# Kernel tuning notes

Measured on AMD Instinct MI355X. Metric: run time of the kernel, lower is better.

The kernel has to match this reference:

```python
import jax, jax.numpy as jnp
import numpy as np

B = 2
G = 256            # bev grid size per axis at this stride
STRIDE = 2
PAD = 2
EMB = 128
NPF = 64           # num_pos_feats = emb_dim // 2
LR = np.array([-51.2, -51.2, -3.0, 51.2, 51.2, 1.0], np.float32)
VS = np.array([0.2, 0.2], np.float32)
OFFSET = -128      # round(lr_min / (voxel * stride))
SQRT_DIM = float(np.sqrt(EMB))
Q = 65536
V = B * G * G


def pos2posemb2d(pos, num_pos_feats=NPF, temperature=10000.0):
    # standard interleaved sin/cos 2d position embedding (y first, then x)
    pos = pos * (2.0 * np.pi)
    dim_t = jnp.arange(num_pos_feats, dtype=jnp.float32)
    dim_t = temperature ** (2.0 * (dim_t // 2) / num_pos_feats)
    px = pos[..., 0:1] / dim_t
    py = pos[..., 1:2] / dim_t
    px = jnp.stack((jnp.sin(px[..., 0::2]), jnp.cos(px[..., 1::2])), axis=-1).reshape(pos.shape[0], -1)
    py = jnp.stack((jnp.sin(py[..., 0::2]), jnp.cos(py[..., 1::2])), axis=-1).reshape(pos.shape[0], -1)
    return jnp.concatenate((py, px), axis=-1)


def mlp(x, w1, b1, w2, b2):
    return jax.nn.relu(x @ w1 + b1) @ w2 + b2


def setup_inputs():
    key = jax.random.key(0)
    ks = jax.random.split(key, 16)
    # dense BEV grid of value centers -> value_map scatter is collision-free
    idx = jnp.arange(V)
    b = idx // (G * G)
    x = (idx % (G * G)) // G
    y = idx % G
    ctr_coor = jnp.stack([b, (x - 128) * STRIDE, (y - 128) * STRIDE], axis=-1).astype(jnp.int32)
    ctr_feat = jax.random.normal(ks[0], (V, EMB), jnp.float32)
    bq = jax.random.randint(ks[1], (Q,), 0, B).astype(jnp.float32)
    xy = jax.random.uniform(ks[2], (Q, 2), jnp.float32, -51.0, 51.0)
    ref_pts = jnp.concatenate([bq[:, None], xy], axis=1)
    s = 0.02
    p = lambda k, sh: jax.random.normal(k, sh, jnp.float32) * s
    return dict(
        ref_pts=ref_pts, ctr_coor=ctr_coor, ctr_feat=ctr_feat,
        q_w1=p(ks[3], (EMB, 2 * EMB)), q_b1=jnp.zeros((2 * EMB,), jnp.float32),
        q_w2=p(ks[4], (2 * EMB, EMB)), q_b2=jnp.zeros((EMB,), jnp.float32),
        v_w1=p(ks[5], (EMB, 2 * EMB)), v_b1=jnp.zeros((2 * EMB,), jnp.float32),
        v_w2=p(ks[6], (2 * EMB, EMB)), v_b2=jnp.zeros((EMB,), jnp.float32),
        se_wr=p(ks[7], (EMB, EMB)), se_br=jnp.zeros((EMB,), jnp.float32),
        se_we=p(ks[8], (EMB, EMB)), se_be=jnp.zeros((EMB,), jnp.float32),
    )


def _forward(ref_pts, ctr_feat, q_w1, q_b1, q_w2, q_b2, v_w1, v_b1, v_w2, v_b2,
             se_wr, se_br, se_we, se_be, ctr_coor):
    nv = ctr_feat.shape[0]
    lr = jnp.asarray(LR)
    vs = jnp.asarray(VS)
    # indices2metric: voxel center positions in meters
    ctr_xy = (ctr_coor[:, 1:].astype(jnp.float32) + 0.5) * vs
    # coor_to_indices: grid indices at current stride
    ctr_inds = ctr_coor[:, 1:] // STRIDE - OFFSET                 # (V,2) in [0,G)
    ref_coor = jnp.floor(ref_pts[:, 1:] / vs)                     # metric2indices
    ref_inds = (ref_coor / STRIDE - OFFSET).astype(jnp.int32)     # (Q,2) in [0,G)
    # normalized positions in [0,1]
    qp = (ref_pts[:, 1:] - lr[0:2]) / (lr[3:5] - lr[0:2])
    vp = (ctr_xy - lr[0:2]) / (lr[3:5] - lr[0:2])
    qpos = mlp(pos2posemb2d(qp), q_w1, q_b1, q_w2, q_b2)          # (Q,d)
    vpos = mlp(pos2posemb2d(vp), v_w1, v_b1, v_w2, v_b2)          # (V,d)
    # SELayer_Linear: gate value pos-emb by features
    gate = jax.nn.sigmoid(jax.nn.relu(ctr_feat @ se_wr + se_br) @ se_we + se_be)
    vpos = vpos * gate
    # build padded index map and gather 3x3 neighborhoods
    vmap_grid = -jnp.ones((B, G + 2 * PAD, G + 2 * PAD), jnp.int32)
    vmap_grid = vmap_grid.at[ctr_coor[:, 0], ctr_inds[:, 0] + PAD, ctr_inds[:, 1] + PAD].set(
        jnp.arange(nv, dtype=jnp.int32))
    r = jnp.arange(-1, 2)
    nbrs = jnp.stack(jnp.meshgrid(r, r, indexing='ij'), axis=-1).reshape(-1, 2)  # (9,2)
    bq = ref_pts[:, 0].astype(jnp.int32)
    nx = ref_inds[:, 0:1] + PAD + nbrs[:, 0]                      # (Q,9)
    ny = ref_inds[:, 1:2] + PAD + nbrs[:, 1]
    v_idx = vmap_grid[bq[:, None], nx, ny] + 1                    # missing -> 0 (padded zero row)
    vpos_pad = jnp.concatenate([jnp.zeros((1, EMB), vpos.dtype), vpos], axis=0)
    feat_pad = jnp.concatenate([jnp.zeros((1, EMB), ctr_feat.dtype), ctr_feat], axis=0)
    score = jnp.einsum('qd,qnd->qn', qpos, vpos_pad[v_idx]) / SQRT_DIM
    attn = jax.nn.softmax(score, axis=-1)
    return jnp.einsum('qn,qnd->qd', attn, feat_pad[v_idx])       # (Q,d)


def reference(ref_pts, ctr_coor, ctr_feat, q_w1, q_b1, q_w2, q_b2,
              v_w1, v_b1, v_w2, v_b2, se_wr, se_br, se_we, se_be):
    return _forward(ref_pts, ctr_feat, q_w1, q_b1, q_w2, q_b2,
                    v_w1, v_b1, v_w2, v_b2, se_wr, se_br, se_we, se_be, ctr_coor)
```

## Files before the change

### kernel.cpp

```cpp
#include <hip/hip_runtime.h>
#include <math.h>

#define TWO_PI 6.28318530717958647692f
#define SCALE_INV_SQRT_D 0.08838834764831844f

#define NQ 65536
#define NV 131072

typedef __attribute__((ext_vector_type(8))) short s16x8;
typedef __attribute__((ext_vector_type(4))) float f32x4;

__device__ __forceinline__ unsigned short f2bf(float f) {
    unsigned int u = __builtin_bit_cast(unsigned int, f);
    u += 0x7fffu + ((u >> 16) & 1u);
    return (unsigned short)(u >> 16);
}

__global__ __launch_bounds__(256) void prep_kernel(
    const float* __restrict__ qw1, const float* __restrict__ qw2,
    const float* __restrict__ vw1, const float* __restrict__ vw2,
    const float* __restrict__ sewr, const float* __restrict__ sewe,
    unsigned short* __restrict__ wbuf)
{
    int i = blockIdx.x * 256 + threadIdx.x;
    const float* src; int K, N, base, li;
    if (i < 32768)       { src = qw1;  K = 128; N = 256; base = 0;      li = i; }
    else if (i < 65536)  { src = qw2;  K = 256; N = 128; base = 32768;  li = i - 32768; }
    else if (i < 98304)  { src = vw1;  K = 128; N = 256; base = 65536;  li = i - 65536; }
    else if (i < 131072) { src = vw2;  K = 256; N = 128; base = 98304;  li = i - 98304; }
    else if (i < 147456) { src = sewr; K = 128; N = 128; base = 131072; li = i - 131072; }
    else                 { src = sewe; K = 128; N = 128; base = 147456; li = i - 147456; }
    int n = li / K, k = li - n * K;
    wbuf[base + li] = f2bf(src[k * N + n]);
}

template<bool GATE>
__global__ __launch_bounds__(256) void mlp_kernel(
    const float* __restrict__ ref_pts,
    const int*   __restrict__ ctr_coor,
    const float* __restrict__ ctr_feat,
    const unsigned short* __restrict__ w1t,
    const float* __restrict__ b1,
    const unsigned short* __restrict__ w2t,
    const float* __restrict__ b2,
    const unsigned short* __restrict__ sewrt,
    const float* __restrict__ sebr,
    const unsigned short* __restrict__ sewet,
    const float* __restrict__ sebe,
    float* __restrict__ outbuf)
{
    __shared__ __attribute__((aligned(16))) unsigned short s_pe[64 * 128];
    __shared__ __attribute__((aligned(16))) unsigned short s_h[64 * 256];
    __shared__ float s_p[128];

    const int t    = threadIdx.x;
    const int lane = t & 63;
    const int wid  = t >> 6;
    const int row0 = blockIdx.x * 64;
    const int r16  = lane & 15;
    const int g    = lane >> 4;

    if (t < 64) {
        int row = row0 + t;
        float xx, yy;
        if (GATE) {
            xx = ((float)ctr_coor[row * 3 + 1] + 0.5f) * 0.2f;
            yy = ((float)ctr_coor[row * 3 + 2] + 0.5f) * 0.2f;
        } else {
            xx = ref_pts[row * 3 + 1];
            yy = ref_pts[row * 3 + 2];
        }
        s_p[t]      = (xx + 51.2f) * (TWO_PI / 102.4f);
        s_p[64 + t] = (yy + 51.2f) * (TWO_PI / 102.4f);
    }
    __syncthreads();

    {
        const int row = t >> 2, q = t & 3;
        const float p = s_p[(q < 2 ? 64 : 0) + row];
        unsigned short vals[32];
        #pragma unroll
        for (int kk = 0; kk < 16; ++kk) {
            int k = (q & 1) * 16 + kk;
            float ang = p * __builtin_exp2f((float)k * -0.41524101186092029f);
            float sn, cs;
            __sincosf(ang, &sn, &cs);
            vals[2 * kk]     = f2bf(sn);
            vals[2 * kk + 1] = f2bf(cs);
        }
        #pragma unroll
        for (int c = 0; c < 4; ++c) {
            int byte = row * 256 + q * 64 + c * 16;
            byte ^= (row & 7) << 4;
            *(s16x8*)((char*)s_pe + byte) = *(const s16x8*)(vals + c * 8);
        }
    }
    __syncthreads();

    {
        const int col0 = wid * 64;
        f32x4 acc[4][4];
        #pragma unroll
        for (int m = 0; m < 4; ++m)
            #pragma unroll
            for (int n = 0; n < 4; ++n) acc[m][n] = (f32x4)0.f;

        #pragma unroll
        for (int ks = 0; ks < 4; ++ks) {
            s16x8 a[4], b[4];
            #pragma unroll
            for (int m = 0; m < 4; ++m) {
                int row = m * 16 + r16;
                int byte = (row * 256 + ks * 64 + g * 16) ^ ((row & 7) << 4);
                a[m] = *(const s16x8*)((const char*)s_pe + byte);
            }
            #pragma unroll
            for (int n = 0; n < 4; ++n) {
                int wrow = col0 + n * 16 + r16;
                b[n] = *(const s16x8*)(w1t + wrow * 128 + ks * 32 + g * 8);
            }
            #pragma unroll
            for (int m = 0; m < 4; ++m)
                #pragma unroll
                for (int n = 0; n < 4; ++n)
                    acc[m][n] = __builtin_amdgcn_mfma_f32_16x16x32_bf16(a[m], b[n], acc[m][n], 0, 0, 0);
        }
        #pragma unroll
        for (int n = 0; n < 4; ++n) {
            const int col = col0 + n * 16 + r16;
            const float bias = b1[col];
            #pragma unroll
            for (int m = 0; m < 4; ++m)
                #pragma unroll
                for (int r = 0; r < 4; ++r) {
                    int row = m * 16 + g * 4 + r;
                    float v = fmaxf(acc[m][n][r] + bias, 0.f);
                    int byte = (row * 512 + col * 2) ^ ((row & 7) << 4);
                    *(unsigned short*)((char*)s_h + byte) = f2bf(v);
                }
        }
    }
    __syncthreads();

    f32x4 c2[4][2];
    #pragma unroll
    for (int m = 0; m < 4; ++m)
        #pragma unroll
        for (int n = 0; n < 2; ++n) c2[m][n] = (f32x4)0.f;
    {
        const int col0 = wid * 32;
        #pragma unroll
        for (int ks = 0; ks < 8; ++ks) {
            s16x8 a[4], b[2];
            #pragma unroll
            for (int m = 0; m < 4; ++m) {
                int row = m * 16 + r16;
                int byte = (row * 512 + ks * 64 + g * 16) ^ ((row & 7) << 4);
                a[m] = *(const s16x8*)((const char*)s_h + byte);
            }
            #pragma unroll
            for (int n = 0; n < 2; ++n) {
                int wrow = col0 + n * 16 + r16;
                b[n] = *(const s16x8*)(w2t + wrow * 256 + ks * 32 + g * 8);
            }
            #pragma unroll
            for (int m = 0; m < 4; ++m)
                #pragma unroll
                for (int n = 0; n < 2; ++n)
                    c2[m][n] = __builtin_amdgcn_mfma_f32_16x16x32_bf16(a[m], b[n], c2[m][n], 0, 0, 0);
        }
    }

    if (!GATE) {
        #pragma unroll
        for (int n = 0; n < 2; ++n) {
            const int col = wid * 32 + n * 16 + r16;
            const float bias = b2[col];
            #pragma unroll
            for (int m = 0; m < 4; ++m)
                #pragma unroll
                for (int r = 0; r < 4; ++r) {
                    int row = row0 + m * 16 + g * 4 + r;
                    outbuf[(size_t)row * 128 + col] = c2[m][n][r] + bias;
                }
        }
        return;
    }

    __syncthreads();
    {
        #pragma unroll
        for (int it = 0; it < 8; ++it) {
            int idx = it * 256 + t;
            int row = idx >> 5;
            int c4  = idx & 31;
            f32x4 v = *(const f32x4*)(ctr_feat + (size_t)(row0 + row) * 128 + c4 * 4);
            unsigned short u[4] = {f2bf(v.x), f2bf(v.y), f2bf(v.z), f2bf(v.w)};
            int byte = (row * 256 + c4 * 8) ^ ((row & 7) << 4);
            *(unsigned long long*)((char*)s_pe + byte) = *(const unsigned long long*)u;
        }
    }
    __syncthreads();

    {
        const int col0 = wid * 32;
        f32x4 acc[4][2];
        #pragma unroll
        for (int m = 0; m < 4; ++m)
            #pragma unroll
            for (int n = 0; n < 2; ++n) acc[m][n] = (f32x4)0.f;
        #pragma unroll
        for (int ks = 0; ks < 4; ++ks) {
            s16x8 a[4], b[2];
            #pragma unroll
            for (int m = 0; m < 4; ++m) {
                int row = m * 16 + r16;
                int byte = (row * 256 + ks * 64 + g * 16) ^ ((row & 7) << 4);
                a[m] = *(const s16x8*)((const char*)s_pe + byte);
            }
            #pragma unroll
            for (int n = 0; n < 2; ++n) {
                int wrow = col0 + n * 16 + r16;
                b[n] = *(const s16x8*)(sewrt + wrow * 128 + ks * 32 + g * 8);
            }
            #pragma unroll
            for (int m = 0; m < 4; ++m)
                #pragma unroll
                for (int n = 0; n < 2; ++n)
                    acc[m][n] = __builtin_amdgcn_mfma_f32_16x16x32_bf16(a[m], b[n], acc[m][n], 0, 0, 0);
        }
        #pragma unroll
        for (int n = 0; n < 2; ++n) {
            const int col = col0 + n * 16 + r16;
            const float bias = sebr[col];
            #pragma unroll
            for (int m = 0; m < 4; ++m)
                #pragma unroll
                for (int r = 0; r < 4; ++r) {
                    int row = m * 16 + g * 4 + r;
                    float v = fmaxf(acc[m][n][r] + bias, 0.f);
                    int byte = (row * 256 + col * 2) ^ ((row & 7) << 4);
                    *(unsigned short*)((char*)s_h + byte) = f2bf(v);
                }
        }
    }
    __syncthreads();

    {
        const int col0 = wid * 32;
        f32x4 acc[4][2];
        #pragma unroll
        for (int m = 0; m < 4; ++m)
            #pragma unroll
            for (int n = 0; n < 2; ++n) acc[m][n] = (f32x4)0.f;
        #pragma unroll
        for (int ks = 0; ks < 4; ++ks) {
            s16x8 a[4], b[2];
            #pragma unroll
            for (int m = 0; m < 4; ++m) {
                int row = m * 16 + r16;
                int byte = (row * 256 + ks * 64 + g * 16) ^ ((row & 7) << 4);
                a[m] = *(const s16x8*)((const char*)s_h + byte);
            }
            #pragma unroll
            for (int n = 0; n < 2; ++n) {
                int wrow = col0 + n * 16 + r16;
                b[n] = *(const s16x8*)(sewet + wrow * 128 + ks * 32 + g * 8);
            }
            #pragma unroll
            for (int m = 0; m < 4; ++m)
                #pragma unroll
                for (int n = 0; n < 2; ++n)
                    acc[m][n] = __builtin_amdgcn_mfma_f32_16x16x32_bf16(a[m], b[n], acc[m][n], 0, 0, 0);
        }
        #pragma unroll
        for (int n = 0; n < 2; ++n) {
            const int col = col0 + n * 16 + r16;
            const float b2v = b2[col];
            const float bev = sebe[col];
            #pragma unroll
            for (int m = 0; m < 4; ++m)
                #pragma unroll
                for (int r = 0; r < 4; ++r) {
                    int row = row0 + m * 16 + g * 4 + r;
                    float gate = 1.0f / (1.0f + __expf(-(acc[m][n][r] + bev)));
                    outbuf[(size_t)row * 128 + col] = (c2[m][n][r] + b2v) * gate;
                }
        }
    }
}

__global__ __launch_bounds__(256) void attn_kernel(
    const float* __restrict__ ref_pts,
    const float* __restrict__ qpos,
    const float* __restrict__ vposg,
    const float* __restrict__ ctr_feat,
    float* __restrict__ out)
{
    const int lane = threadIdx.x & 63;
    const int qi   = blockIdx.x * 4 + (threadIdx.x >> 6);

    const int   b = (int)ref_pts[qi * 3 + 0];
    const float x = ref_pts[qi * 3 + 1];
    const float y = ref_pts[qi * 3 + 2];
    const int xi = (int)(floorf(x / 0.2f) * 0.5f + 128.0f);
    const int yi = (int)(floorf(y / 0.2f) * 0.5f + 128.0f);

    const float2 qv = *(const float2*)(qpos + (size_t)qi * 128 + lane * 2);

    float  sc[9];
    float2 fv[9];
    #pragma unroll
    for (int n = 0; n < 9; ++n) {
        const int nx = xi + n / 3 - 1;
        const int ny = yi + n % 3 - 1;
        const bool valid = ((unsigned)nx < 256u) && ((unsigned)ny < 256u);
        float  s = 0.f;
        float2 f = {0.f, 0.f};
        if (valid) {
            const int idx = (b << 16) + (nx << 8) + ny;
            const float2 v = *(const float2*)(vposg + (size_t)idx * 128 + lane * 2);
            f = *(const float2*)(ctr_feat + (size_t)idx * 128 + lane * 2);
            s = qv.x * v.x + qv.y * v.y;
        }
        sc[n] = s;
        fv[n] = f;
    }

    #pragma unroll
    for (int off = 32; off > 0; off >>= 1) {
        #pragma unroll
        for (int n = 0; n < 9; ++n)
            sc[n] += __shfl_xor(sc[n], off, 64);
    }

    float m = -1e30f;
    #pragma unroll
    for (int n = 0; n < 9; ++n) {
        sc[n] *= SCALE_INV_SQRT_D;
        m = fmaxf(m, sc[n]);
    }
    float e[9], denom = 0.f;
    #pragma unroll
    for (int n = 0; n < 9; ++n) {
        e[n] = __expf(sc[n] - m);
        denom += e[n];
    }
    const float inv = 1.0f / denom;

    float2 o = {0.f, 0.f};
    #pragma unroll
    for (int n = 0; n < 9; ++n) {
        const float w = e[n] * inv;
        o.x += w * fv[n].x;
        o.y += w * fv[n].y;
    }
    *(float2*)(out + (size_t)qi * 128 + lane * 2) = o;
}

extern "C" void kernel_launch(void* const* d_in, const int* in_sizes, int n_in,
                              void* d_out, int out_size, void* d_ws, size_t ws_size,
                              hipStream_t stream) {
    const float* ref_pts  = (const float*)d_in[0];
    const int*   ctr_coor = (const int*)d_in[1];
    const float* ctr_feat = (const float*)d_in[2];
    const float* q_w1 = (const float*)d_in[3];
    const float* q_b1 = (const float*)d_in[4];
    const float* q_w2 = (const float*)d_in[5];
    const float* q_b2 = (const float*)d_in[6];
    const float* v_w1 = (const float*)d_in[7];
    const float* v_b1 = (const float*)d_in[8];
    const float* v_w2 = (const float*)d_in[9];
    const float* v_b2 = (const float*)d_in[10];
    const float* se_wr = (const float*)d_in[11];
    const float* se_br = (const float*)d_in[12];
    const float* se_we = (const float*)d_in[13];
    const float* se_be = (const float*)d_in[14];

    unsigned short* wbuf = (unsigned short*)d_ws;
    float* vposg = (float*)((char*)d_ws + 163840 * 2);
    float* qposb = vposg + (size_t)NV * 128;

    const unsigned short* qw1t  = wbuf;
    const unsigned short* qw2t  = wbuf + 32768;
    const unsigned short* vw1t  = wbuf + 65536;
    const unsigned short* vw2t  = wbuf + 98304;
    const unsigned short* sewrt = wbuf + 131072;
    const unsigned short* sewet = wbuf + 147456;

    prep_kernel<<<640, 256, 0, stream>>>(q_w1, q_w2, v_w1, v_w2, se_wr, se_we, wbuf);

    mlp_kernel<false><<<NQ / 64, 256, 0, stream>>>(
        ref_pts, nullptr, nullptr,
        qw1t, q_b1, qw2t, q_b2,
        nullptr, nullptr, nullptr, nullptr, qposb);

    mlp_kernel<true><<<NV / 64, 256, 0, stream>>>(
        nullptr, ctr_coor, ctr_feat,
        vw1t, v_b1, vw2t, v_b2,
        sewrt, se_br, sewet, se_be, vposg);

    attn_kernel<<<NQ / 4, 256, 0, stream>>>(
        ref_pts, qposb, vposg, ctr_feat, (float*)d_out);
}
```

Before: 202.3 us.

## Restructure MLP kernel to per-wave 16-row tiles with transposed LDS reads, bf16 intermediates

Each wave now owns 16 rows and computes the full chained MLP and gate path independently, keeping layer-1 outputs in a per-wave LDS region. The second GEMM reads that region with ds_read_b64_tr_b16 transposed loads, and the prep kernel permutes the K index of the second-layer weights to match. This removes block-wide __syncthreads between stages. The qpos and vpos intermediates are now stored as bf16, which halves their write and gather traffic in the attention kernel but adds rounding error. Each wave now reloads all weight B-fragments from global memory for only 16 rows, so weight reuse across rows drops.

```diff
diff --git a/kernel.cpp b/kernel.cpp
--- a/kernel.cpp
+++ b/kernel.cpp
@@ -8,12 +8,28 @@
 #define NV 131072
 
 typedef __attribute__((ext_vector_type(8))) short s16x8;
+typedef __attribute__((ext_vector_type(4))) short s16x4;
 typedef __attribute__((ext_vector_type(4))) float f32x4;
 
 __device__ __forceinline__ unsigned short f2bf(float f) {
     unsigned int u = __builtin_bit_cast(unsigned int, f);
     u += 0x7fffu + ((u >> 16) & 1u);
     return (unsigned short)(u >> 16);
+}
+__device__ __forceinline__ float bf2f(unsigned short s) {
+    return __builtin_bit_cast(float, (unsigned)s << 16);
+}
+__device__ __forceinline__ s16x4 ds_tr16(unsigned addr) {
+    s16x4 r;
+    asm volatile("ds_read_b64_tr_b16 %0, %1" : "=v"(r) : "v"(addr) : "memory");
+    return r;
+}
+#define LGKM0() asm volatile("s_waitcnt lgkmcnt(0)" ::: "memory")
+#define SBAR0() __builtin_amdgcn_sched_barrier(0)
+
+__device__ __forceinline__ int kperm(int kk) {
+    int i = kk & 7, gg = (kk >> 3) & 3, ks = kk >> 5;
+    return (ks << 5) + ((i & 4) << 2) + (gg << 2) + (i & 3);
 }
 
 __global__ __launch_bounds__(256) void prep_kernel(
@@ -23,15 +39,14 @@
     unsigned short* __restrict__ wbuf)
 {
     int i = blockIdx.x * 256 + threadIdx.x;
-    const float* src; int K, N, base, li;
-    if (i < 32768)       { src = qw1;  K = 128; N = 256; base = 0;      li = i; }
-    else if (i < 65536)  { src = qw2;  K = 256; N = 128; base = 32768;  li = i - 32768; }
-    else if (i < 98304)  { src = vw1;  K = 128; N = 256; base = 65536;  li = i - 65536; }
-    else if (i < 131072) { src = vw2;  K = 256; N = 128; base = 98304;  li = i - 98304; }
-    else if (i < 147456) { src = sewr; K = 128; N = 128; base = 131072; li = i - 131072; }
-    else                 { src = sewe; K = 128; N = 128; base = 147456; li = i - 147456; }
-    int n = li / K, k = li - n * K;
-    wbuf[base + li] = f2bf(src[k * N + n]);
+    float v;
+    if (i < 32768)        { int li = i;          int n = li >> 7, k = li & 127;          v = qw1[k * 256 + n]; }
+    else if (i < 65536)   { int li = i - 32768;  int n = li >> 8, k = kperm(li & 255);   v = qw2[k * 128 + n]; }
+    else if (i < 98304)   { int li = i - 65536;  int n = li >> 7, k = li & 127;          v = vw1[k * 256 + n]; }
+    else if (i < 131072)  { int li = i - 98304;  int n = li >> 8, k = kperm(li & 255);   v = vw2[k * 128 + n]; }
+    else if (i < 147456)  { int li = i - 131072; int n = li >> 7, k = li & 127;          v = sewr[k * 128 + n]; }
+    else                  { int li = i - 147456; int n = li >> 7, k = kperm(li & 127);   v = sewe[k * 128 + n]; }
+    wbuf[i] = f2bf(v);
 }
 
 template<bool GATE>
@@ -41,259 +56,210 @@
     const float* __restrict__ ctr_feat,
     const unsigned short* __restrict__ w1t,
     const float* __restrict__ b1,
-    const unsigned short* __restrict__ w2t,
+    const unsigned short* __restrict__ w2tp,
     const float* __restrict__ b2,
     const unsigned short* __restrict__ sewrt,
     const float* __restrict__ sebr,
-    const unsigned short* __restrict__ sewet,
+    const unsigned short* __restrict__ sewetp,
     const float* __restrict__ sebe,
-    float* __restrict__ outbuf)
+    unsigned short* __restrict__ outb)
 {
-    __shared__ __attribute__((aligned(16))) unsigned short s_pe[64 * 128];
-    __shared__ __attribute__((aligned(16))) unsigned short s_h[64 * 256];
-    __shared__ float s_p[128];
-
+    __shared__ __attribute__((aligned(16))) char s_lds[32768];
     const int t    = threadIdx.x;
     const int lane = t & 63;
     const int wid  = t >> 6;
-    const int row0 = blockIdx.x * 64;
     const int r16  = lane & 15;
     const int g    = lane >> 4;
-
-    if (t < 64) {
-        int row = row0 + t;
-        float xx, yy;
-        if (GATE) {
-            xx = ((float)ctr_coor[row * 3 + 1] + 0.5f) * 0.2f;
-            yy = ((float)ctr_coor[row * 3 + 2] + 0.5f) * 0.2f;
-        } else {
-            xx = ref_pts[row * 3 + 1];
-            yy = ref_pts[row * 3 + 2];
-        }
-        s_p[t]      = (xx + 51.2f) * (TWO_PI / 102.4f);
-        s_p[64 + t] = (yy + 51.2f) * (TWO_PI / 102.4f);
-    }
-    __syncthreads();
+    const int row0w = blockIdx.x * 64 + wid * 16;
+
+    char* regA = s_lds + wid * 8192;
+    char* regB = regA + 4096;
+    const unsigned bA = (unsigned)(size_t)regA;
+    const unsigned bB = (unsigned)(size_t)regB;
+    const int swz = (r16 & 7) << 4;
+
+    float xx, yy;
+    if (GATE) {
+        xx = ((float)ctr_coor[(row0w + r16) * 3 + 1] + 0.5f) * 0.2f;
+        yy = ((float)ctr_coor[(row0w + r16) * 3 + 2] + 0.5f) * 0.2f;
+    } else {
+        xx = ref_pts[(row0w + r16) * 3 + 1];
+        yy = ref_pts[(row0w + r16) * 3 + 2];
+    }
+    const float px = (xx + 51.2f) * (TWO_PI / 102.4f);
+    const float py = (yy + 51.2f) * (TWO_PI / 102.4f);
+
+    f32x4 gacc[8];
+    if (GATE) {
+        #pragma unroll
+        for (int it = 0; it < 8; ++it) {
+            int row = it * 2 + (lane >> 5);
+            int c4  = lane & 31;
+            f32x4 v = *(const f32x4*)(ctr_feat + (size_t)(row0w + row) * 128 + c4 * 4);
+            unsigned long long pk = (unsigned long long)f2bf(v.x)
+                | ((unsigned long long)f2bf(v.y) << 16)
+                | ((unsigned long long)f2bf(v.z) << 32)
+                | ((unsigned long long)f2bf(v.w) << 48);
+            int byte = (row * 256 + c4 * 8) ^ ((row & 7) << 4);
+            *(unsigned long long*)(regB + byte) = pk;
+        }
+        {
+            s16x8 a[4];
+            #pragma unroll
+            for (int ks = 0; ks < 4; ++ks)
+                a[ks] = *(const s16x8*)(regB + ((r16 * 256 + ks * 64 + g * 16) ^ swz));
+            f32x4 acc[8];
+            #pragma unroll
+            for (int n = 0; n < 8; ++n) acc[n] = (f32x4)0.f;
+            #pragma unroll
+            for (int n = 0; n < 8; ++n)
+                #pragma unroll
+                for (int ks = 0; ks < 4; ++ks) {
+                    s16x8 b = *(const s16x8*)(sewrt + (n * 16 + r16) * 128 + ks * 32 + g * 8);
+                    acc[n] = __builtin_amdgcn_mfma_f32_16x16x32_bf16(a[ks], b, acc[n], 0, 0, 0);
+                }
+            #pragma unroll
+            for (int n = 0; n < 8; ++n) {
+                float bias = sebr[n * 16 + r16];
+                float e0 = fmaxf(acc[n][0] + bias, 0.f);
+                float e1 = fmaxf(acc[n][1] + bias, 0.f);
+                float e2 = fmaxf(acc[n][2] + bias, 0.f);
+                float e3 = fmaxf(acc[n][3] + bias, 0.f);
+                unsigned long long pk = (unsigned long long)f2bf(e0)
+                    | ((unsigned long long)f2bf(e1) << 16)
+                    | ((unsigned long long)f2bf(e2) << 32)
+                    | ((unsigned long long)f2bf(e3) << 48);
+                *(unsigned long long*)(regA + (n * 16 + r16) * 32 + g * 8) = pk;
+            }
+        }
+        {
+            LGKM0();
+            s16x4 lo[4], hi[4];
+            #pragma unroll
+            for (int ks = 0; ks < 4; ++ks) {
+                unsigned ad = bA + ks * 1024 + g * 128 + r16 * 2;
+                lo[ks] = ds_tr16(ad);
+                hi[ks] = ds_tr16(ad + 512);
+            }
+            LGKM0(); SBAR0();
+            s16x8 a[4];
+            #pragma unroll
+            for (int ks = 0; ks < 4; ++ks)
+                a[ks] = __builtin_shufflevector(lo[ks], hi[ks], 0, 1, 2, 3, 4, 5, 6, 7);
+            #pragma unroll
+            for (int n = 0; n < 8; ++n) gacc[n] = (f32x4)0.f;
+            #pragma unroll
+            for (int n = 0; n < 8; ++n)
+                #pragma unroll
+                for (int ks = 0; ks < 4; ++ks) {
+                    s16x8 b = *(const s16x8*)(sewetp + (n * 16 + r16) * 128 + ks * 32 + g * 8);
+                    gacc[n] = __builtin_amdgcn_mfma_f32_16x16x32_bf16(a[ks], b, gacc[n], 0, 0, 0);
+                }
+        }
+    }
 
     {
-        const int row = t >> 2, q = t & 3;
-        const float p = s_p[(q < 2 ? 64 : 0) + row];
-        unsigned short vals[32];
+        const float p = (g < 2) ? py : px;
+        s16x8 pv[4];
         #pragma unroll
         for (int kk = 0; kk < 16; ++kk) {
-            int k = (q & 1) * 16 + kk;
+            int k = (g & 1) * 16 + kk;
             float ang = p * __builtin_exp2f((float)k * -0.41524101186092029f);
             float sn, cs;
             __sincosf(ang, &sn, &cs);
-            vals[2 * kk]     = f2bf(sn);
-            vals[2 * kk + 1] = f2bf(cs);
+            pv[kk >> 2][(kk & 3) * 2]     = (short)f2bf(sn);
+            pv[kk >> 2][(kk & 3) * 2 + 1] = (short)f2bf(cs);
         }
         #pragma unroll
         for (int c = 0; c < 4; ++c) {
-            int byte = row * 256 + q * 64 + c * 16;
-            byte ^= (row & 7) << 4;
-            *(s16x8*)((char*)s_pe + byte) = *(const s16x8*)(vals + c * 8);
-        }
-    }
-    __syncthreads();
-
-    {
-        const int col0 = wid * 64;
-        f32x4 acc[4][4];
-        #pragma unroll
-        for (int m = 0; m < 4; ++m)
-            #pragma unroll
-            for (int n = 0; n < 4; ++n) acc[m][n] = (f32x4)0.f;
-
-        #pragma unroll
-        for (int ks = 0; ks < 4; ++ks) {
-            s16x8 a[4], b[4];
-            #pragma unroll
-            for (int m = 0; m < 4; ++m) {
-                int row = m * 16 + r16;
-                int byte = (row * 256 + ks * 64 + g * 16) ^ ((row & 7) << 4);
-                a[m] = *(const s16x8*)((const char*)s_pe + byte);
-            }
-            #pragma unroll
-            for (int n = 0; n < 4; ++n) {
-                int wrow = col0 + n * 16 + r16;
-                b[n] = *(const s16x8*)(w1t + wrow * 128 + ks * 32 + g * 8);
-            }
-            #pragma unroll
-            for (int m = 0; m < 4; ++m)
+            int byte = (r16 * 256 + g * 64 + c * 16) ^ swz;
+            *(s16x8*)(regA + byte) = pv[c];
+        }
+    }
+
+    f32x4 c2[8];
+    #pragma unroll
+    for (int n = 0; n < 8; ++n) c2[n] = (f32x4)0.f;
+
+    s16x8 ape[4];
+    #pragma unroll
+    for (int ks = 0; ks < 4; ++ks)
+        ape[ks] = *(const s16x8*)(regA + ((r16 * 256 + ks * 64 + g * 16) ^ swz));
+
+    #pragma unroll
+    for (int half = 0; half < 2; ++half) {
+        {
+            f32x4 acc[8];
+            #pragma unroll
+            for (int n = 0; n < 8; ++n) acc[n] = (f32x4)0.f;
+            #pragma unroll
+            for (int n = 0; n < 8; ++n)
                 #pragma unroll
-                for (int n = 0; n < 4; ++n)
-                    acc[m][n] = __builtin_amdgcn_mfma_f32_16x16x32_bf16(a[m], b[n], acc[m][n], 0, 0, 0);
-        }
-        #pragma unroll
-        for (int n = 0; n < 4; ++n) {
-            const int col = col0 + n * 16 + r16;
-            const float bias = b1[col];
-            #pragma unroll
-            for (int m = 0; m < 4; ++m)
+                for (int ks = 0; ks < 4; ++ks) {
+                    s16x8 b = *(const s16x8*)(w1t + (half * 128 + n * 16 + r16) * 128 + ks * 32 + g * 8);
+                    acc[n] = __builtin_amdgcn_mfma_f32_16x16x32_bf16(ape[ks], b, acc[n], 0, 0, 0);
+                }
+            #pragma unroll
+            for (int n = 0; n < 8; ++n) {
+                float bias = b1[half * 128 + n * 16 + r16];
+                float e0 = fmaxf(acc[n][0] + bias, 0.f);
+                float e1 = fmaxf(acc[n][1] + bias, 0.f);
+                float e2 = fmaxf(acc[n][2] + bias, 0.f);
+                float e3 = fmaxf(acc[n][3] + bias, 0.f);
+                unsigned long long pk = (unsigned long long)f2bf(e0)
+                    | ((unsigned long long)f2bf(e1) << 16)
+                    | ((unsigned long long)f2bf(e2) << 32)
+                    | ((unsigned long long)f2bf(e3) << 48);
+                *(unsigned long long*)(regB + (n * 16 + r16) * 32 + g * 8) = pk;
+            }
+        }
+        {
+            LGKM0();
+            s16x4 lo[4], hi[4];
+            #pragma unroll
+            for (int ks = 0; ks < 4; ++ks) {
+                unsigned ad = bB + ks * 1024 + g * 128 + r16 * 2;
+                lo[ks] = ds_tr16(ad);
+                hi[ks] = ds_tr16(ad + 512);
+            }
+            LGKM0(); SBAR0();
+            s16x8 a[4];
+            #pragma unroll
+            for (int ks = 0; ks < 4; ++ks)
+                a[ks] = __builtin_shufflevector(lo[ks], hi[ks], 0, 1, 2, 3, 4, 5, 6, 7);
+            #pragma unroll
+            for (int n = 0; n < 8; ++n)
                 #pragma unroll
-                for (int r = 0; r < 4; ++r) {
-                    int row = m * 16 + g * 4 + r;
-                    float v = fmaxf(acc[m][n][r] + bias, 0.f);
-                    int byte = (row * 512 + col * 2) ^ ((row & 7) << 4);
-                    *(unsigned short*)((char*)s_h + byte) = f2bf(v);
+                for (int ks = 0; ks < 4; ++ks) {
+                    s16x8 b = *(const s16x8*)(w2tp + (n * 16 + r16) * 256 + (half * 4 + ks) * 32 + g * 8);
+                    c2[n] = __builtin_amdgcn_mfma_f32_16x16x32_bf16(a[ks], b, c2[n], 0, 0, 0);
                 }
         }
     }
-    __syncthreads();
-
-    f32x4 c2[4][2];
-    #pragma unroll
-    for (int m = 0; m < 4; ++m)
-        #pragma unroll
-        for (int n = 0; n < 2; ++n) c2[m][n] = (f32x4)0.f;
-    {
-        const int col0 = wid * 32;
-        #pragma unroll
-        for (int ks = 0; ks < 8; ++ks) {
-            s16x8 a[4], b[2];
-            #pragma unroll
-            for (int m = 0; m < 4; ++m) {
-                int row = m * 16 + r16;
-                int byte = (row * 512 + ks * 64 + g * 16) ^ ((row & 7) << 4);
-                a[m] = *(const s16x8*)((const char*)s_h + byte);
-            }
-            #pragma unroll
-            for (int n = 0; n < 2; ++n) {
-                int wrow = col0 + n * 16 + r16;
-                b[n] = *(const s16x8*)(w2t + wrow * 256 + ks * 32 + g * 8);
-            }
-            #pragma unroll
-            for (int m = 0; m < 4; ++m)
-                #pragma unroll
-                for (int n = 0; n < 2; ++n)
-                    c2[m][n] = __builtin_amdgcn_mfma_f32_16x16x32_bf16(a[m], b[n], c2[m][n], 0, 0, 0);
-        }
-    }
-
-    if (!GATE) {
-        #pragma unroll
-        for (int n = 0; n < 2; ++n) {
-            const int col = wid * 32 + n * 16 + r16;
-            const float bias = b2[col];
-            #pragma unroll
-            for (int m = 0; m < 4; ++m)
-                #pragma unroll
-                for (int r = 0; r < 4; ++r) {
-                    int row = row0 + m * 16 + g * 4 + r;
-                    outbuf[(size_t)row * 128 + col] = c2[m][n][r] + bias;
-                }
-        }
-        return;
-    }
-
-    __syncthreads();
-    {
-        #pragma unroll
-        for (int it = 0; it < 8; ++it) {
-            int idx = it * 256 + t;
-            int row = idx >> 5;
-            int c4  = idx & 31;
-            f32x4 v = *(const f32x4*)(ctr_feat + (size_t)(row0 + row) * 128 + c4 * 4);
-            unsigned short u[4] = {f2bf(v.x), f2bf(v.y), f2bf(v.z), f2bf(v.w)};
-            int byte = (row * 256 + c4 * 8) ^ ((row & 7) << 4);
-            *(unsigned long long*)((char*)s_pe + byte) = *(const unsigned long long*)u;
-        }
-    }
-    __syncthreads();
-
-    {
-        const int col0 = wid * 32;
-        f32x4 acc[4][2];
-        #pragma unroll
-        for (int m = 0; m < 4; ++m)
-            #pragma unroll
-            for (int n = 0; n < 2; ++n) acc[m][n] = (f32x4)0.f;
-        #pragma unroll
-        for (int ks = 0; ks < 4; ++ks) {
-            s16x8 a[4], b[2];
-            #pragma unroll
-            for (int m = 0; m < 4; ++m) {
-                int row = m * 16 + r16;
-                int byte = (row * 256 + ks * 64 + g * 16) ^ ((row & 7) << 4);
-                a[m] = *(const s16x8*)((const char*)s_pe + byte);
-            }
-            #pragma unroll
-            for (int n = 0; n < 2; ++n) {
-                int wrow = col0 + n * 16 + r16;
-                b[n] = *(const s16x8*)(sewrt + wrow * 128 + ks * 32 + g * 8);
-            }
-            #pragma unroll
-            for (int m = 0; m < 4; ++m)
-                #pragma unroll
-                for (int n = 0; n < 2; ++n)
-                    acc[m][n] = __builtin_amdgcn_mfma_f32_16x16x32_bf16(a[m], b[n], acc[m][n], 0, 0, 0);
-        }
-        #pragma unroll
-        for (int n = 0; n < 2; ++n) {
-            const int col = col0 + n * 16 + r16;
-            const float bias = sebr[col];
-            #pragma unroll
-            for (int m = 0; m < 4; ++m)
-                #pragma unroll
-                for (int r = 0; r < 4; ++r) {
-                    int row = m * 16 + g * 4 + r;
-                    float v = fmaxf(acc[m][n][r] + bias, 0.f);
-                    int byte = (row * 256 + col * 2) ^ ((row & 7) << 4);
-                    *(unsigned short*)((char*)s_h + byte) = f2bf(v);
-                }
-        }
-    }
-    __syncthreads();
-
-    {
-        const int col0 = wid * 32;
-        f32x4 acc[4][2];
-        #pragma unroll
-        for (int m = 0; m < 4; ++m)
-            #pragma unroll
-            for (int n = 0; n < 2; ++n) acc[m][n] = (f32x4)0.f;
-        #pragma unroll
-        for (int ks = 0; ks < 4; ++ks) {
-            s16x8 a[4], b[2];
-            #pragma unroll
-            for (int m = 0; m < 4; ++m) {
-                int row = m * 16 + r16;
-                int byte = (row * 256 + ks * 64 + g * 16) ^ ((row & 7) << 4);
-                a[m] = *(const s16x8*)((const char*)s_h + byte);
-            }
-            #pragma unroll
-            for (int n = 0; n < 2; ++n) {
-                int wrow = col0 + n * 16 + r16;
-                b[n] = *(const s16x8*)(sewet + wrow * 128 + ks * 32 + g * 8);
-            }
-            #pragma unroll
-            for (int m = 0; m < 4; ++m)
-                #pragma unroll
-                for (int n = 0; n < 2; ++n)
-                    acc[m][n] = __builtin_amdgcn_mfma_f32_16x16x32_bf16(a[m], b[n], acc[m][n], 0, 0, 0);
-        }
-        #pragma unroll
-        for (int n = 0; n < 2; ++n) {
-            const int col = col0 + n * 16 + r16;
-            const float b2v = b2[col];
-            const float bev = sebe[col];
-            #pragma unroll
-            for (int m = 0; m < 4; ++m)
-                #pragma unroll
-                for (int r = 0; r < 4; ++r) {
-                    int row = row0 + m * 16 + g * 4 + r;
-                    float gate = 1.0f / (1.0f + __expf(-(acc[m][n][r] + bev)));
-                    outbuf[(size_t)row * 128 + col] = (c2[m][n][r] + b2v) * gate;
-                }
+
+    #pragma unroll
+    for (int n = 0; n < 8; ++n) {
+        int col = n * 16 + r16;
+        float b2v = b2[col];
+        if (GATE) {
+            float bev = sebe[col];
+            #pragma unroll
+            for (int r = 0; r < 4; ++r) {
+                float gate = 1.0f / (1.0f + __expf(-(gacc[n][r] + bev)));
+                outb[(size_t)(row0w + g * 4 + r) * 128 + col] = f2bf((c2[n][r] + b2v) * gate);
+            }
+        } else {
+            #pragma unroll
+            for (int r = 0; r < 4; ++r)
+                outb[(size_t)(row0w + g * 4 + r) * 128 + col] = f2bf(c2[n][r] + b2v);
         }
     }
 }
 
 __global__ __launch_bounds__(256) void attn_kernel(
     const float* __restrict__ ref_pts,
-    const float* __restrict__ qpos,
-    const float* __restrict__ vposg,
+    const unsigned short* __restrict__ qpos,
+    const unsigned short* __restrict__ vposg,
     const float* __restrict__ ctr_feat,
     float* __restrict__ out)
 {
@@ -306,7 +272,9 @@
     const int xi = (int)(floorf(x / 0.2f) * 0.5f + 128.0f);
     const int yi = (int)(floorf(y / 0.2f) * 0.5f + 128.0f);
 
-    const float2 qv = *(const float2*)(qpos + (size_t)qi * 128 + lane * 2);
+    const unsigned qp = *(const unsigned*)(qpos + (size_t)qi * 128 + lane * 2);
+    const float qx = bf2f((unsigned short)(qp & 0xffffu));
+    const float qy = bf2f((unsigned short)(qp >> 16));
 
     float  sc[9];
     float2 fv[9];
@@ -319,9 +287,9 @@
         float2 f = {0.f, 0.f};
         if (valid) {
             const int idx = (b << 16) + (nx << 8) + ny;
-            const float2 v = *(const float2*)(vposg + (size_t)idx * 128 + lane * 2);
+            const unsigned vp = *(const unsigned*)(vposg + (size_t)idx * 128 + lane * 2);
             f = *(const float2*)(ctr_feat + (size_t)idx * 128 + lane * 2);
-            s = qv.x * v.x + qv.y * v.y;
+            s = qx * bf2f((unsigned short)(vp & 0xffffu)) + qy * bf2f((unsigned short)(vp >> 16));
         }
         sc[n] = s;
         fv[n] = f;
@@ -377,28 +345,28 @@
     const float* se_we = (const float*)d_in[13];
     const float* se_be = (const float*)d_in[14];
 
-    unsigned short* wbuf = (unsigned short*)d_ws;
-    float* vposg = (float*)((char*)d_ws + 163840 * 2);
-    float* qposb = vposg + (size_t)NV * 128;
-
-    const unsigned short* qw1t  = wbuf;
-    const unsigned short* qw2t  = wbuf + 32768;
-    const unsigned short* vw1t  = wbuf + 65536;
-    const unsigned short* vw2t  = wbuf + 98304;
-    const unsigned short* sewrt = wbuf + 131072;
-    const unsigned short* sewet = wbuf + 147456;
+    unsigned short* wbuf  = (unsigned short*)d_ws;
+    unsigned short* vposg = wbuf + 163840;
+    unsigned short* qposb = vposg + (size_t)NV * 128;
+
+    const unsigned short* qw1t   = wbuf;
+    const unsigned short* qw2tp  = wbuf + 32768;
+    const unsigned short* vw1t   = wbuf + 65536;
+    const unsigned short* vw2tp  = wbuf + 98304;
+    const unsigned short* sewrt  = wbuf + 131072;
+    const unsigned short* sewetp = wbuf + 147456;
 
     prep_kernel<<<640, 256, 0, stream>>>(q_w1, q_w2, v_w1, v_w2, se_wr, se_we, wbuf);
 
     mlp_kernel<false><<<NQ / 64, 256, 0, stream>>>(
         ref_pts, nullptr, nullptr,
-        qw1t, q_b1, qw2t, q_b2,
+        qw1t, q_b1, qw2tp, q_b2,
         nullptr, nullptr, nullptr, nullptr, qposb);
 
     mlp_kernel<true><<<NV / 64, 256, 0, stream>>>(
         nullptr, ctr_coor, ctr_feat,
-        vw1t, v_b1, vw2t, v_b2,
-        sewrt, se_br, sewet, se_be, vposg);
+        vw1t, v_b1, vw2tp, v_b2,
+        sewrt, se_br, sewetp, se_be, vposg);
 
     attn_kernel<<<NQ / 4, 256, 0, stream>>>(
         ref_pts, qposb, vposg, ctr_feat, (float*)d_out);
```

After: 321.5 us. 1.59x slower.
